# Kernel optimization log

Hardware: AMD Instinct MI355X
Metric: run time of the kernel (lower is better)

Reference implementation:

```python
import jax, jax.numpy as jnp
import numpy as np

N = 10000      # nodes
E = 320000     # edges (avg degree 32)
D_IN = 128     # input feature dim
D_H = 256      # hidden dim
L = 3          # num GIN layers


def setup_inputs() -> dict:
    key = jax.random.key(0)
    ks = jax.random.split(key, 2 + 4 * L)
    inp = {
        "x": jax.random.normal(ks[0], (N, D_IN), dtype=jnp.float32),
        "edge_index": jax.random.randint(ks[1], (2, E), 0, N, dtype=jnp.int64),
    }
    din = D_IN
    for l in range(L):
        k1, k2, k3, k4 = ks[2 + 4 * l: 6 + 4 * l]
        s1 = 1.0 / np.sqrt(din)
        s2 = 1.0 / np.sqrt(D_H)
        inp[f"w1_{l}"] = jax.random.uniform(k1, (din, D_H), jnp.float32, -s1, s1)
        inp[f"b1_{l}"] = jax.random.uniform(k2, (D_H,), jnp.float32, -s1, s1)
        inp[f"w2_{l}"] = jax.random.uniform(k3, (D_H, D_H), jnp.float32, -s2, s2)
        inp[f"b2_{l}"] = jax.random.uniform(k4, (D_H,), jnp.float32, -s2, s2)
        din = D_H
    return inp


def reference(x, edge_index,
              w1_0, b1_0, w2_0, b2_0,
              w1_1, b1_1, w2_1, b2_1,
              w1_2, b1_2, w2_2, b2_2):
    src, dst = edge_index[0], edge_index[1]
    layers = [(w1_0, b1_0, w2_0, b2_0),
              (w1_1, b1_1, w2_1, b2_1),
              (w1_2, b1_2, w2_2, b2_2)]
    z = x
    for w1, b1, w2, b2 in layers:
        # GINConv with eps=0: h_i = z_i + sum_{j->i} z_j, then 2-layer MLP
        agg = jax.ops.segment_sum(z[src], dst, num_segments=N)  # [N, d]
        h = z + agg
        h = jax.nn.relu(h @ w1 + b1) @ w2 + b2  # nn.Sequential(Linear, ReLU, Linear)
        z = jax.nn.relu(h)                      # Encoder activation
    return z
```

## Files before the change

### kernel.cpp

```cpp
#include <hip/hip_runtime.h>
#include <hip/hip_bf16.h>
#include <cstdint>


#define NNODES 10000
#define NEDGES 320000
#define DIN 128
#define DH 256

typedef __bf16 bf16x8 __attribute__((ext_vector_type(8)));
typedef unsigned short ushort8v __attribute__((ext_vector_type(8)));
typedef unsigned short ushort4v __attribute__((ext_vector_type(4)));
typedef float f32x4 __attribute__((ext_vector_type(4)));

__device__ __forceinline__ unsigned short f2bf(float f) {
    unsigned int u = __float_as_uint(f);
    unsigned int r = u + 0x7fffu + ((u >> 16) & 1u);
    return (unsigned short)(r >> 16);
}
__device__ __forceinline__ float bf2f(unsigned short u) {
    return __uint_as_float(((unsigned int)u) << 16);
}

struct PrepArgs {
    const float* wsrc[6];
    unsigned short* wdst[6];
    int wkbits[6];
    const int* eb;
    int* flag;
    int* cnt;
    const float* x;
    unsigned short* xb;
};
#define PREP_ZERO_B 40
#define PREP_XCONV_B 1250
#define PREP_WCONV_B 352
#define PREP_GRID (PREP_ZERO_B + 1 + PREP_XCONV_B + PREP_WCONV_B)

__global__ void prep_kernel(PrepArgs a) {
    __shared__ float tile[32][33];
    __shared__ int any;
    int bid = blockIdx.x;
    int tid = threadIdx.x;
    if (bid < PREP_ZERO_B) {
        int i = bid * 256 + tid;
        if (i < NNODES) a.cnt[i] = 0;
    } else if (bid == PREP_ZERO_B) {
        if (tid == 0) any = 0;
        __syncthreads();
        for (int i = tid; i < 1024; i += 256)
            if (a.eb[2 * i + 1] != 0) any = 1;
        __syncthreads();
        if (tid == 0) a.flag[0] = any;
    } else if (bid < PREP_ZERO_B + 1 + PREP_XCONV_B) {
        int i = (bid - PREP_ZERO_B - 1) * 256 + tid;
        if (i < NNODES * DIN / 4) {
            float4 v = reinterpret_cast<const float4*>(a.x)[i];
            ushort4v o = {f2bf(v.x), f2bf(v.y), f2bf(v.z), f2bf(v.w)};
            reinterpret_cast<ushort4v*>(a.xb)[i] = o;
        }
    } else {
        int wb = bid - (PREP_ZERO_B + 1 + PREP_XCONV_B);
        int m, t32;
        if (wb < 32) { m = 0; t32 = wb; }
        else { m = 1 + (wb - 32) / 64; t32 = (wb - 32) % 64; }
        int kb = a.wkbits[m];
        int K = 1 << kb;
        int tc = t32 & 7, tr = t32 >> 3;
        int r = tid >> 3, c4 = (tid & 7) * 4;
        float4 v = *reinterpret_cast<const float4*>(
            &a.wsrc[m][(size_t)(tr * 32 + r) * 256 + tc * 32 + c4]);
        tile[r][c4 + 0] = v.x; tile[r][c4 + 1] = v.y;
        tile[r][c4 + 2] = v.z; tile[r][c4 + 3] = v.w;
        __syncthreads();
        int cc = tid >> 3, k4 = (tid & 7) * 4;
        ushort4v o = {f2bf(tile[k4 + 0][cc]), f2bf(tile[k4 + 1][cc]),
                      f2bf(tile[k4 + 2][cc]), f2bf(tile[k4 + 3][cc])};
        *reinterpret_cast<ushort4v*>(
            &a.wdst[m][(size_t)(tc * 32 + cc) * K + tr * 32 + k4]) = o;
    }
}

__device__ __forceinline__ int eload(const int* __restrict__ eb, int is32, long logical_idx) {
    return is32 ? eb[logical_idx] : eb[2 * logical_idx];
}

__global__ void hist_kernel(const int* __restrict__ eb, const int* __restrict__ flag,
                            int* __restrict__ cnt, int E) {
    int i = blockIdx.x * blockDim.x + threadIdx.x;
    if (i >= E) return;
    int is32 = flag[0];
    int d = eload(eb, is32, (long)E + i);
    atomicAdd(&cnt[d], 1);
}

__global__ __launch_bounds__(1024) void scan_kernel(const int* __restrict__ cnt,
                                                    int* __restrict__ offs,
                                                    int* __restrict__ cursor, int n) {
    __shared__ int sums[1024];
    int tid = threadIdx.x;
    int per = (n + 1023) / 1024;
    int beg = tid * per;
    int local[16];
    int s = 0;
    for (int i = 0; i < per; ++i) {
        int idx = beg + i;
        int v = (idx < n) ? cnt[idx] : 0;
        local[i] = s;
        s += v;
    }
    sums[tid] = s;
    __syncthreads();
    for (int d = 1; d < 1024; d <<= 1) {
        int y = (tid >= d) ? sums[tid - d] : 0;
        __syncthreads();
        sums[tid] += y;
        __syncthreads();
    }
    int base = sums[tid] - s;
    for (int i = 0; i < per; ++i) {
        int idx = beg + i;
        if (idx < n) {
            int v = base + local[i];
            offs[idx] = v;
            cursor[idx] = v;
        }
    }
    if (tid == 1023) offs[n] = sums[1023];
}

__global__ void scatter_kernel(const int* __restrict__ eb, const int* __restrict__ flag,
                               int* __restrict__ cursor, int* __restrict__ srcs, int E) {
    int i = blockIdx.x * blockDim.x + threadIdx.x;
    if (i >= E) return;
    int is32 = flag[0];
    int s = eload(eb, is32, (long)i);
    int d = eload(eb, is32, (long)E + i);
    int pos = atomicAdd(&cursor[d], 1);
    srcs[pos] = s;
}

template <int D>
__global__ __launch_bounds__(256) void agg_add_sliced_kernel(const unsigned short* __restrict__ z,
                                                             const int* __restrict__ srcs,
                                                             const int* __restrict__ offs,
                                                             unsigned short* __restrict__ h, int n) {
    constexpr int NSLICE = (D * 2) / 128;
    constexpr int LPN = 8;
    constexpr int NPB = 256 / LPN;
    int bid = blockIdx.x;
    int slice = bid & (NSLICE - 1);
    int ng = bid / NSLICE;
    int t = threadIdx.x;
    int node = ng * NPB + t / LPN;
    if (node >= n) return;
    int li = t % LPN;
    int col8 = slice * LPN + li;
    const ushort8v* zb = reinterpret_cast<const ushort8v*>(z);
    const int ld8 = D / 8;
    int beg = offs[node], end = offs[node + 1];

    float a0[8] = {}, a1[8] = {}, a2[8] = {}, a3[8] = {};
    int e = beg;
    for (; e + 4 <= end; e += 4) {
        int s0 = srcs[e], s1 = srcs[e + 1], s2 = srcs[e + 2], s3 = srcs[e + 3];
        ushort8v v0 = zb[(size_t)s0 * ld8 + col8];
        ushort8v v1 = zb[(size_t)s1 * ld8 + col8];
        ushort8v v2 = zb[(size_t)s2 * ld8 + col8];
        ushort8v v3 = zb[(size_t)s3 * ld8 + col8];
#pragma unroll
        for (int j = 0; j < 8; ++j) {
            a0[j] += bf2f(v0[j]);
            a1[j] += bf2f(v1[j]);
            a2[j] += bf2f(v2[j]);
            a3[j] += bf2f(v3[j]);
        }
    }
    for (; e < end; ++e) {
        ushort8v v = zb[(size_t)srcs[e] * ld8 + col8];
#pragma unroll
        for (int j = 0; j < 8; ++j) a0[j] += bf2f(v[j]);
    }
    ushort8v zr = zb[(size_t)node * ld8 + col8];
    ushort8v o;
#pragma unroll
    for (int j = 0; j < 8; ++j) {
        float v = a0[j] + a1[j] + a2[j] + a3[j] + bf2f(zr[j]);
        o[j] = f2bf(v);
    }
    reinterpret_cast<ushort8v*>(h)[(size_t)node * ld8 + col8] = o;
}

template <int K, int OUT_BF16>
__global__ __launch_bounds__(512) void mlp_fused_kernel(const unsigned short* __restrict__ A,
                                                        const unsigned short* __restrict__ Wt1,
                                                        const float* __restrict__ b1,
                                                        const unsigned short* __restrict__ Wt2,
                                                        const float* __restrict__ b2,
                                                        void* __restrict__ C, int M) {
    constexpr int NK = K / 32;
    constexpr int NST1 = K / 128;
    __shared__ unsigned short As[NK][4][64][8];
    __shared__ unsigned short Bs[4][4][256][8];
    __shared__ unsigned short Ts[8][4][64][8];
    int tid = threadIdx.x;
    int wave = tid >> 6, lane = tid & 63;
    int strip = wave & 3, chalf = wave >> 2;
    int m0 = blockIdx.x * 64;
    int fr = lane & 15;
    int kc = lane >> 4;

    f32x4 acc[8];
#pragma unroll
    for (int c = 0; c < 8; ++c) acc[c] = (f32x4){0.f, 0.f, 0.f, 0.f};

    {
        int row = tid >> 3, c0 = tid & 7;
        int gr = m0 + row;
#pragma unroll
        for (int i = 0; i < K / 64; ++i) {
            int chunk = c0 + i * 8;
            ushort8v av = {0, 0, 0, 0, 0, 0, 0, 0};
            if (gr < M) av = *reinterpret_cast<const ushort8v*>(&A[(size_t)gr * K + chunk * 8]);
            *reinterpret_cast<ushort8v*>(&As[chunk >> 2][chunk & 3][row][0]) = av;
        }
    }
    int scol = tid >> 2;
    int sscn = tid & 3;

#pragma unroll
    for (int st = 0; st < NST1; ++st) {
#pragma unroll
        for (int cp = 0; cp < 2; ++cp) {
            int c = cp * 128 + scol;
#pragma unroll
            for (int kk = 0; kk < 4; ++kk)
                *reinterpret_cast<ushort8v*>(&Bs[kk][sscn][c][0]) =
                    *reinterpret_cast<const ushort8v*>(&Wt1[(size_t)c * K + st * 128 + kk * 32 + sscn * 8]);
        }
        __syncthreads();
#pragma unroll
        for (int kk = 0; kk < 4; ++kk) {
            bf16x8 af = __builtin_bit_cast(bf16x8,
                *reinterpret_cast<const ushort8v*>(&As[st * 4 + kk][kc][strip * 16 + fr][0]));
#pragma unroll
            for (int c = 0; c < 8; ++c) {
                bf16x8 bf = __builtin_bit_cast(bf16x8,
                    *reinterpret_cast<const ushort8v*>(&Bs[kk][kc][chalf * 128 + c * 16 + fr][0]));
                acc[c] = __builtin_amdgcn_mfma_f32_16x16x32_bf16(af, bf, acc[c], 0, 0, 0);
            }
        }
        __syncthreads();
    }
#pragma unroll
    for (int cf = 0; cf < 8; ++cf) {
        int col = chalf * 128 + cf * 16 + fr;
        float bb = b1[col];
#pragma unroll
        for (int j = 0; j < 4; ++j) {
            int row = strip * 16 + kc * 4 + j;
            float v = fmaxf(acc[cf][j] + bb, 0.f);
            Ts[col >> 5][(col >> 3) & 3][row][col & 7] = f2bf(v);
        }
        acc[cf] = (f32x4){0.f, 0.f, 0.f, 0.f};
    }

#pragma unroll
    for (int st = 0; st < 2; ++st) {
#pragma unroll
        for (int cp = 0; cp < 2; ++cp) {
            int c = cp * 128 + scol;
#pragma unroll
            for (int kk = 0; kk < 4; ++kk)
                *reinterpret_cast<ushort8v*>(&Bs[kk][sscn][c][0]) =
                    *reinterpret_cast<const ushort8v*>(&Wt2[(size_t)c * 256 + st * 128 + kk * 32 + sscn * 8]);
        }
        __syncthreads();
#pragma unroll
        for (int kk = 0; kk < 4; ++kk) {
            bf16x8 af = __builtin_bit_cast(bf16x8,
                *reinterpret_cast<const ushort8v*>(&Ts[st * 4 + kk][kc][strip * 16 + fr][0]));
#pragma unroll
            for (int c = 0; c < 8; ++c) {
                bf16x8 bf = __builtin_bit_cast(bf16x8,
                    *reinterpret_cast<const ushort8v*>(&Bs[kk][kc][chalf * 128 + c * 16 + fr][0]));
                acc[c] = __builtin_amdgcn_mfma_f32_16x16x32_bf16(af, bf, acc[c], 0, 0, 0);
            }
        }
        __syncthreads();
    }
#pragma unroll
    for (int cf = 0; cf < 8; ++cf) {
        int col = chalf * 128 + cf * 16 + fr;
        float bb = b2[col];
#pragma unroll
        for (int j = 0; j < 4; ++j) {
            int row = m0 + strip * 16 + kc * 4 + j;
            if (row < M) {
                float v = fmaxf(acc[cf][j] + bb, 0.f);
                if (OUT_BF16)
                    ((unsigned short*)C)[(size_t)row * 256 + col] = f2bf(v);
                else
                    ((float*)C)[(size_t)row * 256 + col] = v;
            }
        }
    }
}

extern "C" void kernel_launch(void* const* d_in, const int* in_sizes, int n_in,
                              void* d_out, int out_size, void* d_ws, size_t ws_size,
                              hipStream_t stream) {
    const float* x = (const float*)d_in[0];
    const int* eb = (const int*)d_in[1];
    const int E = NEDGES;
    const int N = NNODES;

    const float* w1[3] = {(const float*)d_in[2], (const float*)d_in[6], (const float*)d_in[10]};
    const float* b1[3] = {(const float*)d_in[3], (const float*)d_in[7], (const float*)d_in[11]};
    const float* w2[3] = {(const float*)d_in[4], (const float*)d_in[8], (const float*)d_in[12]};
    const float* b2[3] = {(const float*)d_in[5], (const float*)d_in[9], (const float*)d_in[13]};

    char* ws = (char*)d_ws;
    size_t off = 0;
    auto alloc = [&](size_t bytes) {
        void* p = ws + off;
        off += (bytes + 255) & ~(size_t)255;
        return p;
    };
    int* flag   = (int*)alloc(4);
    int* cnt    = (int*)alloc((size_t)N * 4);
    int* offs   = (int*)alloc((size_t)(N + 1) * 4);
    int* cursor = (int*)alloc((size_t)N * 4);
    int* srcs   = (int*)alloc((size_t)E * 4);
    unsigned short* xb   = (unsigned short*)alloc((size_t)N * DIN * 2);
    unsigned short* zbuf = (unsigned short*)alloc((size_t)N * DH * 2);
    unsigned short* hbuf = (unsigned short*)alloc((size_t)N * DH * 2);
    unsigned short* wt[6];
    wt[0] = (unsigned short*)alloc((size_t)DIN * DH * 2);
    for (int i = 1; i < 6; ++i) wt[i] = (unsigned short*)alloc((size_t)DH * DH * 2);
    (void)ws_size; (void)n_in; (void)out_size; (void)in_sizes;

    PrepArgs pa;
    pa.wsrc[0] = w1[0]; pa.wsrc[1] = w2[0]; pa.wsrc[2] = w1[1];
    pa.wsrc[3] = w2[1]; pa.wsrc[4] = w1[2]; pa.wsrc[5] = w2[2];
    for (int i = 0; i < 6; ++i) pa.wdst[i] = wt[i];
    pa.wkbits[0] = 7;
    for (int i = 1; i < 6; ++i) pa.wkbits[i] = 8;
    pa.eb = eb; pa.flag = flag; pa.cnt = cnt; pa.x = x; pa.xb = xb;
    prep_kernel<<<PREP_GRID, 256, 0, stream>>>(pa);

    hist_kernel<<<(E + 255) / 256, 256, 0, stream>>>(eb, flag, cnt, E);
    scan_kernel<<<1, 1024, 0, stream>>>(cnt, offs, cursor, N);
    scatter_kernel<<<(E + 255) / 256, 256, 0, stream>>>(eb, flag, cursor, srcs, E);

    int mlp_grid = (N + 63) / 64;
    int agg_blocks_256 = ((N + 31) / 32) * 4;
    int agg_blocks_128 = ((N + 31) / 32) * 2;

    agg_add_sliced_kernel<128><<<agg_blocks_128, 256, 0, stream>>>(xb, srcs, offs, hbuf, N);
    mlp_fused_kernel<128, 1><<<mlp_grid, 512, 0, stream>>>(hbuf, wt[0], b1[0], wt[1], b2[0], zbuf, N);

    agg_add_sliced_kernel<256><<<agg_blocks_256, 256, 0, stream>>>(zbuf, srcs, offs, hbuf, N);
    mlp_fused_kernel<256, 1><<<mlp_grid, 512, 0, stream>>>(hbuf, wt[2], b1[1], wt[3], b2[1], zbuf, N);

    agg_add_sliced_kernel<256><<<agg_blocks_256, 256, 0, stream>>>(zbuf, srcs, offs, hbuf, N);
    mlp_fused_kernel<256, 0><<<mlp_grid, 512, 0, stream>>>(hbuf, wt[4], b1[2], wt[5], b2[2], (float*)d_out, N);
}
```

Measured before the change: 152.0 us.

## Use 2x4 wave MFMA tiling in fused MLP and warp-shuffle scan

The fused MLP kernel moves from each wave owning a 16-row by 128-column strip to a 2x4 wave grid where each wave computes a 32x64 tile. Each wave now loads 2 A fragments and 4 B fragments per k-step instead of 1 and 8, which cuts LDS reads per MFMA. Separately, the prefix-scan kernel replaces a 1024-entry shared-memory Hillis-Steele scan, with two barriers per step, by wave-level shuffle scans plus a small cross-wave scan. Both aim to reduce LDS traffic and synchronisation; the scan is a small part of the total run time.

```diff
diff --git a/kernel.cpp b/kernel.cpp
--- a/kernel.cpp
+++ b/kernel.cpp
@@ -97,8 +97,8 @@
 __global__ __launch_bounds__(1024) void scan_kernel(const int* __restrict__ cnt,
                                                     int* __restrict__ offs,
                                                     int* __restrict__ cursor, int n) {
-    __shared__ int sums[1024];
-    int tid = threadIdx.x;
+    __shared__ int wsums[16];
+    int tid = threadIdx.x, lane = tid & 63, wid = tid >> 6;
     int per = (n + 1023) / 1024;
     int beg = tid * per;
     int local[16];
@@ -109,15 +109,24 @@
         local[i] = s;
         s += v;
     }
-    sums[tid] = s;
+    int inc = s;
+    for (int d = 1; d < 64; d <<= 1) {
+        int y = __shfl_up(inc, d, 64);
+        if (lane >= d) inc += y;
+    }
+    if (lane == 63) wsums[wid] = inc;
     __syncthreads();
-    for (int d = 1; d < 1024; d <<= 1) {
-        int y = (tid >= d) ? sums[tid - d] : 0;
-        __syncthreads();
-        sums[tid] += y;
-        __syncthreads();
-    }
-    int base = sums[tid] - s;
+    if (tid < 16) {
+        int v = wsums[tid];
+        for (int d = 1; d < 16; d <<= 1) {
+            int y = __shfl_up(v, d, 64);
+            if (tid >= d) v += y;
+        }
+        wsums[tid] = v;
+    }
+    __syncthreads();
+    int wbase = (wid > 0) ? wsums[wid - 1] : 0;
+    int base = wbase + inc - s;
     for (int i = 0; i < per; ++i) {
         int idx = beg + i;
         if (idx < n) {
@@ -126,7 +135,7 @@
             cursor[idx] = v;
         }
     }
-    if (tid == 1023) offs[n] = sums[1023];
+    if (tid == 1023) offs[n] = wbase + inc;
 }
 
 __global__ void scatter_kernel(const int* __restrict__ eb, const int* __restrict__ flag,
@@ -205,14 +214,16 @@
     __shared__ unsigned short Ts[8][4][64][8];
     int tid = threadIdx.x;
     int wave = tid >> 6, lane = tid & 63;
-    int strip = wave & 3, chalf = wave >> 2;
+    int wr = wave >> 2, wc = wave & 3;
     int m0 = blockIdx.x * 64;
     int fr = lane & 15;
     int kc = lane >> 4;
 
-    f32x4 acc[8];
-#pragma unroll
-    for (int c = 0; c < 8; ++c) acc[c] = (f32x4){0.f, 0.f, 0.f, 0.f};
+    f32x4 acc[2][4];
+#pragma unroll
+    for (int i = 0; i < 2; ++i)
+#pragma unroll
+        for (int j = 0; j < 4; ++j) acc[i][j] = (f32x4){0.f, 0.f, 0.f, 0.f};
 
     {
         int row = tid >> 3, c0 = tid & 7;
@@ -241,29 +252,36 @@
         __syncthreads();
 #pragma unroll
         for (int kk = 0; kk < 4; ++kk) {
-            bf16x8 af = __builtin_bit_cast(bf16x8,
-                *reinterpret_cast<const ushort8v*>(&As[st * 4 + kk][kc][strip * 16 + fr][0]));
-#pragma unroll
-            for (int c = 0; c < 8; ++c) {
+            bf16x8 af[2];
+#pragma unroll
+            for (int i = 0; i < 2; ++i)
+                af[i] = __builtin_bit_cast(bf16x8,
+                    *reinterpret_cast<const ushort8v*>(&As[st * 4 + kk][kc][wr * 32 + i * 16 + fr][0]));
+#pragma unroll
+            for (int j = 0; j < 4; ++j) {
                 bf16x8 bf = __builtin_bit_cast(bf16x8,
-                    *reinterpret_cast<const ushort8v*>(&Bs[kk][kc][chalf * 128 + c * 16 + fr][0]));
-                acc[c] = __builtin_amdgcn_mfma_f32_16x16x32_bf16(af, bf, acc[c], 0, 0, 0);
+                    *reinterpret_cast<const ushort8v*>(&Bs[kk][kc][wc * 64 + j * 16 + fr][0]));
+#pragma unroll
+                for (int i = 0; i < 2; ++i)
+                    acc[i][j] = __builtin_amdgcn_mfma_f32_16x16x32_bf16(af[i], bf, acc[i][j], 0, 0, 0);
             }
         }
         __syncthreads();
     }
 #pragma unroll
-    for (int cf = 0; cf < 8; ++cf) {
-        int col = chalf * 128 + cf * 16 + fr;
-        float bb = b1[col];
+    for (int i = 0; i < 2; ++i)
 #pragma unroll
         for (int j = 0; j < 4; ++j) {
-            int row = strip * 16 + kc * 4 + j;
-            float v = fmaxf(acc[cf][j] + bb, 0.f);
-            Ts[col >> 5][(col >> 3) & 3][row][col & 7] = f2bf(v);
-        }
-        acc[cf] = (f32x4){0.f, 0.f, 0.f, 0.f};
-    }
+            int col = wc * 64 + j * 16 + fr;
+            float bb = b1[col];
+#pragma unroll
+            for (int jj = 0; jj < 4; ++jj) {
+                int row = wr * 32 + i * 16 + kc * 4 + jj;
+                float v = fmaxf(acc[i][j][jj] + bb, 0.f);
+                Ts[col >> 5][(col >> 3) & 3][row][col & 7] = f2bf(v);
+            }
+            acc[i][j] = (f32x4){0.f, 0.f, 0.f, 0.f};
+        }
 
 #pragma unroll
     for (int st = 0; st < 2; ++st) {
@@ -278,33 +296,40 @@
         __syncthreads();
 #pragma unroll
         for (int kk = 0; kk < 4; ++kk) {
-            bf16x8 af = __builtin_bit_cast(bf16x8,
-                *reinterpret_cast<const ushort8v*>(&Ts[st * 4 + kk][kc][strip * 16 + fr][0]));
-#pragma unroll
-            for (int c = 0; c < 8; ++c) {
+            bf16x8 af[2];
+#pragma unroll
+            for (int i = 0; i < 2; ++i)
+                af[i] = __builtin_bit_cast(bf16x8,
+                    *reinterpret_cast<const ushort8v*>(&Ts[st * 4 + kk][kc][wr * 32 + i * 16 + fr][0]));
+#pragma unroll
+            for (int j = 0; j < 4; ++j) {
                 bf16x8 bf = __builtin_bit_cast(bf16x8,
-                    *reinterpret_cast<const ushort8v*>(&Bs[kk][kc][chalf * 128 + c * 16 + fr][0]));
-                acc[c] = __builtin_amdgcn_mfma_f32_16x16x32_bf16(af, bf, acc[c], 0, 0, 0);
+                    *reinterpret_cast<const ushort8v*>(&Bs[kk][kc][wc * 64 + j * 16 + fr][0]));
+#pragma unroll
+                for (int i = 0; i < 2; ++i)
+                    acc[i][j] = __builtin_amdgcn_mfma_f32_16x16x32_bf16(af[i], bf, acc[i][j], 0, 0, 0);
             }
         }
         __syncthreads();
     }
 #pragma unroll
-    for (int cf = 0; cf < 8; ++cf) {
-        int col = chalf * 128 + cf * 16 + fr;
-        float bb = b2[col];
+    for (int i = 0; i < 2; ++i)
 #pragma unroll
         for (int j = 0; j < 4; ++j) {
-            int row = m0 + strip * 16 + kc * 4 + j;
-            if (row < M) {
-                float v = fmaxf(acc[cf][j] + bb, 0.f);
-                if (OUT_BF16)
-                    ((unsigned short*)C)[(size_t)row * 256 + col] = f2bf(v);
-                else
-                    ((float*)C)[(size_t)row * 256 + col] = v;
+            int col = wc * 64 + j * 16 + fr;
+            float bb = b2[col];
+#pragma unroll
+            for (int jj = 0; jj < 4; ++jj) {
+                int row = m0 + wr * 32 + i * 16 + kc * 4 + jj;
+                if (row < M) {
+                    float v = fmaxf(acc[i][j][jj] + bb, 0.f);
+                    if (OUT_BF16)
+                        ((unsigned short*)C)[(size_t)row * 256 + col] = f2bf(v);
+                    else
+                        ((float*)C)[(size_t)row * 256 + col] = v;
+                }
             }
         }
-    }
 }
 
 extern "C" void kernel_launch(void* const* d_in, const int* in_sizes, int n_in,
```

Measured after the change: 146.7 us. 3.5% less time.
